# Kernel tuning notes

Measured on AMD Instinct MI355X. Metric: run time of the kernel, lower is better.

The kernel has to match this reference:

```python
import jax, jax.numpy as jnp
import numpy as np

EMBED_DIM = 768
FF_MULT = 4
HIDDEN = EMBED_DIM * FF_MULT
BATCH, SEQ = 32, 1024
EPS = 1e-6


def rmsnorm(x, g):
    # RMSNorm over last dim with learned scale g
    return x * jax.lax.rsqrt(jnp.mean(x * x, axis=-1, keepdims=True) + EPS) * g


def act_quant(x):
    # per-token int8 absmax quantization (BitNet b1.58)
    scale = 127.0 / jnp.clip(jnp.max(jnp.abs(x), axis=-1, keepdims=True), 1e-5, None)
    return jnp.clip(jnp.round(x * scale), -128.0, 127.0) / scale


def weight_quant(w):
    # per-tensor ternary (1.58-bit) absmean quantization
    scale = 1.0 / jnp.clip(jnp.mean(jnp.abs(w)), 1e-5, None)
    return jnp.clip(jnp.round(w * scale), -1.0, 1.0) / scale


def bitlinear(x, w, g):
    xn = rmsnorm(x, g)
    # straight-through estimator: forward uses quantized values
    xq = xn + jax.lax.stop_gradient(act_quant(xn) - xn)
    wq = w + jax.lax.stop_gradient(weight_quant(w) - w)
    return jnp.einsum('bsd,fd->bsf', xq, wq)


def setup_inputs() -> dict:
    key = jax.random.key(0)
    k1, k2, k3 = jax.random.split(key, 3)
    x = jax.random.normal(k1, (BATCH, SEQ, EMBED_DIM), dtype=jnp.float32)
    w1 = jax.random.normal(k2, (HIDDEN, EMBED_DIM), dtype=jnp.float32) * 0.02
    w2 = jax.random.normal(k3, (EMBED_DIM, HIDDEN), dtype=jnp.float32) * 0.02
    g1 = jnp.ones((EMBED_DIM,), dtype=jnp.float32)
    g2 = jnp.ones((HIDDEN,), dtype=jnp.float32)
    return {"x": x, "w1": w1, "g1": g1, "w2": w2, "g2": g2}


def reference(x, w1, g1, w2, g2):
    # BitFeedForward: BitLinear -> GELU (exact, matches nn.GELU) -> BitLinear
    # Dropout(p=0.0) is identity.
    h = jax.nn.gelu(bitlinear(x, w1, g1), approximate=False)
    return bitlinear(h, w2, g2)
```

## Files before the change

### kernel.cpp

```cpp
#include <hip/hip_runtime.h>
#include <hip/hip_bf16.h>
#include <hip/hip_fp16.h>
#include <math.h>

#define TOKENS 32768
#define EMBED  768
#define HIDDEN 3072
#define WELEMS (EMBED*HIDDEN)

typedef __attribute__((ext_vector_type(4))) int i32x4;
typedef __attribute__((ext_vector_type(4))) signed char i8x4;
typedef signed char i8;

__device__ __forceinline__ float wave_reduce_sum(float v) {
    for (int o = 32; o > 0; o >>= 1) v += __shfl_down(v, o);
    return v;
}
__device__ __forceinline__ float wave_reduce_max(float v) {
    for (int o = 32; o > 0; o >>= 1) v = fmaxf(v, __shfl_down(v, o));
    return v;
}

__device__ __forceinline__ float gelu_fast(float v) {
    const float z  = fabsf(v) * 0.70710678118654752440f;
    const float t  = __builtin_amdgcn_rcpf(fmaf(0.3275911f, z, 1.0f));
    float p = fmaf(1.061405429f, t, -1.453152027f);
    p = fmaf(p, t, 1.421413741f);
    p = fmaf(p, t, -0.284496736f);
    p = fmaf(p, t, 0.254829592f);
    p = p * t;
    const float e   = __expf(-z * z);
    const float erf = fmaf(-p, e, 1.0f);
    const float se  = (v >= 0.f) ? erf : -erf;
    return 0.5f * v * (1.0f + se);
}

__global__ __launch_bounds__(256) void k_abs_partial(const float* __restrict__ w,
                                                     float* __restrict__ out, int n) {
    float s = 0.f;
    for (int i = blockIdx.x * 256 + threadIdx.x; i < n; i += gridDim.x * 256)
        s += fabsf(w[i]);
    __shared__ float red[4];
    s = wave_reduce_sum(s);
    if ((threadIdx.x & 63) == 0) red[threadIdx.x >> 6] = s;
    __syncthreads();
    if (threadIdx.x == 0) out[blockIdx.x] = red[0] + red[1] + red[2] + red[3];
}

__global__ __launch_bounds__(256) void k_finalize(const float* __restrict__ p,
                                                  float* __restrict__ m) {
    __shared__ float r1[4], r2[4];
    float s1 = 0.f, s2 = 0.f;
    for (int i = threadIdx.x; i < 512; i += 256) { s1 += p[i]; s2 += p[512 + i]; }
    s1 = wave_reduce_sum(s1); s2 = wave_reduce_sum(s2);
    if ((threadIdx.x & 63) == 0) { r1[threadIdx.x >> 6] = s1; r2[threadIdx.x >> 6] = s2; }
    __syncthreads();
    if (threadIdx.x == 0) {
        float m1 = (r1[0] + r1[1] + r1[2] + r1[3]) / (float)WELEMS;
        float m2 = (r2[0] + r2[1] + r2[2] + r2[3]) / (float)WELEMS;
        m[0] = fmaxf(m1, 1e-5f);
        m[1] = fmaxf(m2, 1e-5f);
    }
}

__global__ __launch_bounds__(256) void k_quant_w(const float* __restrict__ w,
                                                 i8* __restrict__ wq,
                                                 const float* __restrict__ mp, int n) {
    const float inv = 1.0f / mp[0];
    for (int i = blockIdx.x * 256 + threadIdx.x; i < n; i += gridDim.x * 256) {
        float q = rintf(w[i] * inv);
        q = fminf(1.f, fmaxf(-1.f, q));
        wq[i] = (i8)(int)q;
    }
}

template <int D>
__global__ __launch_bounds__(256) void k_rms_quant_f32(const float* __restrict__ x,
                                                       const float* __restrict__ g,
                                                       i8* __restrict__ xq,
                                                       float* __restrict__ sc) {
    constexpr int NV = D / 4;
    constexpr int IT = (NV + 255) / 256;
    __shared__ float reds[4], redm[4];
    const int t = blockIdx.x;
    const float4* xp = reinterpret_cast<const float4*>(x + (size_t)t * D);
    const float4* gp = reinterpret_cast<const float4*>(g);
    float4 xg[IT];
    float ssq = 0.f, amax = 0.f;
#pragma unroll
    for (int i = 0; i < IT; ++i) {
        const int idx = i * 256 + (int)threadIdx.x;
        const bool act = (NV % 256 == 0) || (idx < NV);
        if (act) {
            float4 v = xp[idx];
            float4 gv = gp[idx];
            ssq += v.x * v.x + v.y * v.y + v.z * v.z + v.w * v.w;
            xg[i].x = v.x * gv.x; xg[i].y = v.y * gv.y;
            xg[i].z = v.z * gv.z; xg[i].w = v.w * gv.w;
            amax = fmaxf(amax, fmaxf(fmaxf(fabsf(xg[i].x), fabsf(xg[i].y)),
                                     fmaxf(fabsf(xg[i].z), fabsf(xg[i].w))));
        } else {
            xg[i].x = xg[i].y = xg[i].z = xg[i].w = 0.f;
        }
    }
    ssq = wave_reduce_sum(ssq);
    amax = wave_reduce_max(amax);
    if ((threadIdx.x & 63) == 0) { reds[threadIdx.x >> 6] = ssq; redm[threadIdx.x >> 6] = amax; }
    __syncthreads();
    const float S = reds[0] + reds[1] + reds[2] + reds[3];
    const float A = fmaxf(fmaxf(redm[0], redm[1]), fmaxf(redm[2], redm[3]));
    const float rs = (float)(1.0 / sqrt((double)S / D + 1e-6));
    const float an = fmaxf(A * rs, 1e-5f);
    const float qs = rs * (127.0f / an);
    if (threadIdx.x == 0) sc[t] = an * (1.0f / 127.0f);
    i8x4* op = reinterpret_cast<i8x4*>(xq + (size_t)t * D);
#pragma unroll
    for (int i = 0; i < IT; ++i) {
        const int idx = i * 256 + (int)threadIdx.x;
        const bool act = (NV % 256 == 0) || (idx < NV);
        if (act) {
            i8x4 r;
            r[0] = (i8)(int)fminf(127.f, fmaxf(-128.f, rintf(xg[i].x * qs)));
            r[1] = (i8)(int)fminf(127.f, fmaxf(-128.f, rintf(xg[i].y * qs)));
            r[2] = (i8)(int)fminf(127.f, fmaxf(-128.f, rintf(xg[i].z * qs)));
            r[3] = (i8)(int)fminf(127.f, fmaxf(-128.f, rintf(xg[i].w * qs)));
            op[idx] = r;
        }
    }
}

template <int D>
__global__ __launch_bounds__(256) void k_rms_quant_f16(const __half* __restrict__ x,
                                                       const float* __restrict__ g,
                                                       i8* __restrict__ xq,
                                                       float* __restrict__ sc) {
    constexpr int NV = D / 8;
    constexpr int IT = (NV + 255) / 256;
    __shared__ float reds[4], redm[4];
    const int t = blockIdx.x;
    const int4* xp = reinterpret_cast<const int4*>(x + (size_t)t * D);
    const float4* gp = reinterpret_cast<const float4*>(g);
    float xg[IT][8];
    float ssq = 0.f, amax = 0.f;
#pragma unroll
    for (int i = 0; i < IT; ++i) {
        const int idx = i * 256 + (int)threadIdx.x;
        const bool act = (NV % 256 == 0) || (idx < NV);
        if (act) {
            int4 raw = xp[idx];
            const __half2* hp = reinterpret_cast<const __half2*>(&raw);
            float4 g0 = gp[idx * 2];
            float4 g1 = gp[idx * 2 + 1];
            float gv[8] = {g0.x, g0.y, g0.z, g0.w, g1.x, g1.y, g1.z, g1.w};
#pragma unroll
            for (int j = 0; j < 4; ++j) {
                float2 f = __half22float2(hp[j]);
                float a0 = f.x, a1 = f.y;
                ssq += a0 * a0 + a1 * a1;
                xg[i][j * 2]     = a0 * gv[j * 2];
                xg[i][j * 2 + 1] = a1 * gv[j * 2 + 1];
                amax = fmaxf(amax, fmaxf(fabsf(xg[i][j * 2]), fabsf(xg[i][j * 2 + 1])));
            }
        } else {
#pragma unroll
            for (int j = 0; j < 8; ++j) xg[i][j] = 0.f;
        }
    }
    ssq = wave_reduce_sum(ssq);
    amax = wave_reduce_max(amax);
    if ((threadIdx.x & 63) == 0) { reds[threadIdx.x >> 6] = ssq; redm[threadIdx.x >> 6] = amax; }
    __syncthreads();
    const float S = reds[0] + reds[1] + reds[2] + reds[3];
    const float A = fmaxf(fmaxf(redm[0], redm[1]), fmaxf(redm[2], redm[3]));
    const float rs = (float)(1.0 / sqrt((double)S / D + 1e-6));
    const float an = fmaxf(A * rs, 1e-5f);
    const float qs = rs * (127.0f / an);
    if (threadIdx.x == 0) sc[t] = an * (1.0f / 127.0f);
    i8x4* op = reinterpret_cast<i8x4*>(xq + (size_t)t * D);
#pragma unroll
    for (int i = 0; i < IT; ++i) {
        const int idx = i * 256 + (int)threadIdx.x;
        const bool act = (NV % 256 == 0) || (idx < NV);
        if (act) {
            i8x4 r0, r1;
#pragma unroll
            for (int j = 0; j < 4; ++j)
                r0[j] = (i8)(int)fminf(127.f, fmaxf(-128.f, rintf(xg[i][j] * qs)));
#pragma unroll
            for (int j = 0; j < 4; ++j)
                r1[j] = (i8)(int)fminf(127.f, fmaxf(-128.f, rintf(xg[i][4 + j] * qs)));
            op[idx * 2]     = r0;
            op[idx * 2 + 1] = r1;
        }
    }
}

template <bool GELU, typename OutT>
__global__ __launch_bounds__(512, 4) void k_gemm_i8(const i8* __restrict__ A,
                                                    const i8* __restrict__ B,
                                                    OutT* __restrict__ C,
                                                    const float* __restrict__ rsc,
                                                    const float* __restrict__ msc,
                                                    int nbx, int N, int K) {
    __shared__ i8 As[128 * 128];
    __shared__ i8 Bs[256 * 128];
    const int nwg = (int)gridDim.x;
    const int id  = (int)blockIdx.x;
    const int q = nwg >> 3, r = nwg & 7;
    const int xcd = id & 7, sub = id >> 3;
    const int swz = (xcd < r ? xcd * (q + 1) : r * (q + 1) + (xcd - r) * q) + sub;
    const int bx = swz % nbx;
    const int by = swz / nbx;

    const int tid  = threadIdx.x;
    const int lane = tid & 63;
    const int wave = tid >> 6;
    const int wr = wave >> 2, wc = wave & 3;
    const size_t rowBase = (size_t)by * 128;
    const size_t colBase = (size_t)bx * 256;
    const float ms = msc[0];

    i32x4 acc[4][4] = {};

    const int srow = tid >> 3;
    const int cc   = tid & 7;
    const int gcol = (cc ^ (srow & 7)) * 16;
    const i8* gA0 = A + (rowBase + srow) * (size_t)K + gcol;
    const i8* gB0 = B + (colBase + srow) * (size_t)K + gcol;
    const int lOff = srow * 128 + cc * 16;

    const int frow = lane & 15;
    const int fko  = (lane >> 4) * 16;
    const int rswz = (frow & 7) << 4;

    for (int k0 = 0; k0 < K; k0 += 128) {
#pragma unroll
        for (int r2 = 0; r2 < 2; ++r2)
            __builtin_amdgcn_global_load_lds(
                (const __attribute__((address_space(1))) void*)(gA0 + (size_t)r2 * 64 * K + k0),
                (__attribute__((address_space(3))) void*)(&As[lOff + r2 * 64 * 128]), 16, 0, 0);
#pragma unroll
        for (int r4 = 0; r4 < 4; ++r4)
            __builtin_amdgcn_global_load_lds(
                (const __attribute__((address_space(1))) void*)(gB0 + (size_t)r4 * 64 * K + k0),
                (__attribute__((address_space(3))) void*)(&Bs[lOff + r4 * 64 * 128]), 16, 0, 0);
        __syncthreads();
#pragma unroll
        for (int ks = 0; ks < 2; ++ks) {
            i32x4 af[4], bv[4];
#pragma unroll
            for (int mi = 0; mi < 4; ++mi)
                af[mi] = *(const i32x4*)(&As[(wr * 64 + mi * 16 + frow) * 128
                                             + ((ks * 64 + fko) ^ rswz)]);
#pragma unroll
            for (int ni = 0; ni < 4; ++ni)
                bv[ni] = *(const i32x4*)(&Bs[(wc * 64 + ni * 16 + frow) * 128
                                             + ((ks * 64 + fko) ^ rswz)]);
#pragma unroll
            for (int mi = 0; mi < 4; ++mi)
#pragma unroll
                for (int ni = 0; ni < 4; ++ni)
                    acc[mi][ni] = __builtin_amdgcn_mfma_i32_16x16x64_i8(
                        af[mi], bv[ni], acc[mi][ni], 0, 0, 0);
        }
        __syncthreads();
    }

    const int ccol = lane & 15;
    const int crg  = lane >> 4;
#pragma unroll
    for (int mi = 0; mi < 4; ++mi) {
#pragma unroll
        for (int i = 0; i < 4; ++i) {
            size_t row = rowBase + wr * 64 + mi * 16 + crg * 4 + i;
            float rscale = rsc[row] * ms;
#pragma unroll
            for (int ni = 0; ni < 4; ++ni) {
                size_t col = colBase + wc * 64 + ni * 16 + ccol;
                float v = (float)acc[mi][ni][i] * rscale;
                if (GELU) v = gelu_fast(v);
                C[row * (size_t)N + col] = (OutT)v;
            }
        }
    }
}

extern "C" void kernel_launch(void* const* d_in, const int* in_sizes, int n_in,
                              void* d_out, int out_size, void* d_ws, size_t ws_size,
                              hipStream_t stream) {
    const float* x  = (const float*)d_in[0];
    const float* w1 = (const float*)d_in[1];
    const float* g1 = (const float*)d_in[2];
    const float* w2 = (const float*)d_in[3];
    const float* g2 = (const float*)d_in[4];
    float* out = (float*)d_out;

    char* ws = (char*)d_ws;
    float* partials = (float*)ws;
    float* mvals    = (float*)(ws + 4096);
    float* a        = (float*)(ws + 4352);
    float* b        = (float*)(ws + 135424);
    i8*    wq1      = (i8*)(ws + 266496);
    i8*    wq2      = (i8*)(ws + 2625792);
    const size_t FIXED = 4985088;
    char* chunkMem = ws + FIXED;

    const size_t PER_TOK = 768 + 6144 + 3072;
    size_t avail = (ws_size > FIXED) ? (ws_size - FIXED) : 0;
    long long ch = (long long)(avail / PER_TOK);
    ch &= ~255LL;
    if (ch < 256) ch = 256;
    if (ch > TOKENS) ch = TOKENS;
    const int CH = (int)ch;

    k_abs_partial<<<512, 256, 0, stream>>>(w1, partials, WELEMS);
    k_abs_partial<<<512, 256, 0, stream>>>(w2, partials + 512, WELEMS);
    k_finalize<<<1, 256, 0, stream>>>(partials, mvals);
    k_quant_w<<<2048, 256, 0, stream>>>(w1, wq1, mvals + 0, WELEMS);
    k_quant_w<<<2048, 256, 0, stream>>>(w2, wq2, mvals + 1, WELEMS);

    for (int base = 0; base < TOKENS; base += CH) {
        const int rows = (TOKENS - base < CH) ? (TOKENS - base) : CH;
        i8*     xqc = (i8*)chunkMem;
        __half* hc  = (__half*)(chunkMem + (size_t)CH * 768);
        i8*     hqc = (i8*)(chunkMem + (size_t)CH * 768 + (size_t)CH * 6144);

        const int nby = rows / 128;
        const int nbx1 = HIDDEN / 256;
        const int nbx2 = EMBED / 256;

        k_rms_quant_f32<EMBED><<<rows, 256, 0, stream>>>(
            x + (size_t)base * EMBED, g1, xqc, a + base);
        k_gemm_i8<true, __half><<<nbx1 * nby, 512, 0, stream>>>(
            xqc, wq1, hc, a + base, mvals + 0, nbx1, HIDDEN, EMBED);
        k_rms_quant_f16<HIDDEN><<<rows, 256, 0, stream>>>(
            hc, g2, hqc, b + base);
        k_gemm_i8<false, float><<<nbx2 * nby, 512, 0, stream>>>(
            hqc, wq2, out + (size_t)base * EMBED, b + base, mvals + 1, nbx2, EMBED, HIDDEN);
    }
}
```

Measured before the change: 365.2 us.

## Double-buffer int8 GEMM LDS tiles with 128x128 blocks and 256 threads

```diff
diff --git a/kernel.cpp b/kernel.cpp
--- a/kernel.cpp
+++ b/kernel.cpp
@@ -196,14 +196,15 @@
 }
 
 template <bool GELU, typename OutT>
-__global__ __launch_bounds__(512, 4) void k_gemm_i8(const i8* __restrict__ A,
+__global__ __launch_bounds__(256, 2) void k_gemm_i8(const i8* __restrict__ A,
                                                     const i8* __restrict__ B,
                                                     OutT* __restrict__ C,
                                                     const float* __restrict__ rsc,
                                                     const float* __restrict__ msc,
                                                     int nbx, int N, int K) {
-    __shared__ i8 As[128 * 128];
-    __shared__ i8 Bs[256 * 128];
+    __shared__ i8 As[2][128 * 128];
+    __shared__ i8 Bs[2][128 * 128];
+
     const int nwg = (int)gridDim.x;
     const int id  = (int)blockIdx.x;
     const int q = nwg >> 3, r = nwg & 7;
@@ -215,9 +216,9 @@
     const int tid  = threadIdx.x;
     const int lane = tid & 63;
     const int wave = tid >> 6;
-    const int wr = wave >> 2, wc = wave & 3;
+    const int wr = wave >> 1, wc = wave & 1;
     const size_t rowBase = (size_t)by * 128;
-    const size_t colBase = (size_t)bx * 256;
+    const size_t colBase = (size_t)bx * 128;
     const float ms = msc[0];
 
     i32x4 acc[4][4] = {};
@@ -233,38 +234,59 @@
     const int fko  = (lane >> 4) * 16;
     const int rswz = (frow & 7) << 4;
 
-    for (int k0 = 0; k0 < K; k0 += 128) {
-#pragma unroll
-        for (int r2 = 0; r2 < 2; ++r2)
-            __builtin_amdgcn_global_load_lds(
-                (const __attribute__((address_space(1))) void*)(gA0 + (size_t)r2 * 64 * K + k0),
-                (__attribute__((address_space(3))) void*)(&As[lOff + r2 * 64 * 128]), 16, 0, 0);
-#pragma unroll
-        for (int r4 = 0; r4 < 4; ++r4)
-            __builtin_amdgcn_global_load_lds(
-                (const __attribute__((address_space(1))) void*)(gB0 + (size_t)r4 * 64 * K + k0),
-                (__attribute__((address_space(3))) void*)(&Bs[lOff + r4 * 64 * 128]), 16, 0, 0);
-        __syncthreads();
+    const int nt = K >> 7;
+
+#define STAGE(kk, buf)                                                                   \
+    {                                                                                    \
+        const int _k0 = (kk) << 7;                                                       \
+        _Pragma("unroll")                                                                \
+        for (int _r = 0; _r < 4; ++_r) {                                                 \
+            __builtin_amdgcn_global_load_lds(                                            \
+                (const __attribute__((address_space(1))) void*)(gA0 + (size_t)_r * 32 * K + _k0), \
+                (__attribute__((address_space(3))) void*)(&As[buf][lOff + _r * 32 * 128]), 16, 0, 0); \
+            __builtin_amdgcn_global_load_lds(                                            \
+                (const __attribute__((address_space(1))) void*)(gB0 + (size_t)_r * 32 * K + _k0), \
+                (__attribute__((address_space(3))) void*)(&Bs[buf][lOff + _r * 32 * 128]), 16, 0, 0); \
+        }                                                                                \
+    }
+
+    STAGE(0, 0);
+
+    for (int t = 0; t < nt; ++t) {
+        const int cur = t & 1;
+        if (t + 1 < nt) {
+            STAGE(t + 1, cur ^ 1);
+            asm volatile("s_waitcnt vmcnt(8)" ::: "memory");
+        } else {
+            asm volatile("s_waitcnt vmcnt(0)" ::: "memory");
+        }
+        __builtin_amdgcn_s_barrier();
+        __builtin_amdgcn_sched_barrier(0);
 #pragma unroll
         for (int ks = 0; ks < 2; ++ks) {
             i32x4 af[4], bv[4];
 #pragma unroll
             for (int mi = 0; mi < 4; ++mi)
-                af[mi] = *(const i32x4*)(&As[(wr * 64 + mi * 16 + frow) * 128
-                                             + ((ks * 64 + fko) ^ rswz)]);
+                af[mi] = *(const i32x4*)(&As[cur][(wr * 64 + mi * 16 + frow) * 128
+                                                  + ((ks * 64 + fko) ^ rswz)]);
 #pragma unroll
             for (int ni = 0; ni < 4; ++ni)
-                bv[ni] = *(const i32x4*)(&Bs[(wc * 64 + ni * 16 + frow) * 128
-                                             + ((ks * 64 + fko) ^ rswz)]);
+                bv[ni] = *(const i32x4*)(&Bs[cur][(wc * 64 + ni * 16 + frow) * 128
+                                                  + ((ks * 64 + fko) ^ rswz)]);
+            __builtin_amdgcn_s_setprio(1);
 #pragma unroll
             for (int mi = 0; mi < 4; ++mi)
 #pragma unroll
                 for (int ni = 0; ni < 4; ++ni)
                     acc[mi][ni] = __builtin_amdgcn_mfma_i32_16x16x64_i8(
                         af[mi], bv[ni], acc[mi][ni], 0, 0, 0);
-        }
-        __syncthreads();
-    }
+            __builtin_amdgcn_s_setprio(0);
+        }
+        __builtin_amdgcn_sched_barrier(0);
+        __builtin_amdgcn_s_barrier();
+        __builtin_amdgcn_sched_barrier(0);
+    }
+#undef STAGE
 
     const int ccol = lane & 15;
     const int crg  = lane >> 4;
@@ -326,16 +348,16 @@
         i8*     hqc = (i8*)(chunkMem + (size_t)CH * 768 + (size_t)CH * 6144);
 
         const int nby = rows / 128;
-        const int nbx1 = HIDDEN / 256;
-        const int nbx2 = EMBED / 256;
+        const int nbx1 = HIDDEN / 128;
+        const int nbx2 = EMBED / 128;
 
         k_rms_quant_f32<EMBED><<<rows, 256, 0, stream>>>(
             x + (size_t)base * EMBED, g1, xqc, a + base);
-        k_gemm_i8<true, __half><<<nbx1 * nby, 512, 0, stream>>>(
+        k_gemm_i8<true, __half><<<nbx1 * nby, 256, 0, stream>>>(
             xqc, wq1, hc, a + base, mvals + 0, nbx1, HIDDEN, EMBED);
         k_rms_quant_f16<HIDDEN><<<rows, 256, 0, stream>>>(
             hc, g2, hqc, b + base);
-        k_gemm_i8<false, float><<<nbx2 * nby, 512, 0, stream>>>(
+        k_gemm_i8<false, float><<<nbx2 * nby, 256, 0, stream>>>(
             hqc, wq2, out + (size_t)base * EMBED, b + base, mvals + 1, nbx2, EMBED, HIDDEN);
     }
 }
```

Result: slower. 392.8 us (+7.5%).

## Double-buffer int8 GEMM with 256x256 tiles and phased MFMA/load interleaving

Applied to the files above, without the earlier changes.

```diff
diff --git a/kernel.cpp b/kernel.cpp
--- a/kernel.cpp
+++ b/kernel.cpp
@@ -196,83 +196,138 @@
 }
 
 template <bool GELU, typename OutT>
-__global__ __launch_bounds__(512, 4) void k_gemm_i8(const i8* __restrict__ A,
-                                                    const i8* __restrict__ B,
-                                                    OutT* __restrict__ C,
-                                                    const float* __restrict__ rsc,
-                                                    const float* __restrict__ msc,
-                                                    int nbx, int N, int K) {
-    __shared__ i8 As[128 * 128];
-    __shared__ i8 Bs[256 * 128];
+__global__ __launch_bounds__(512, 2) void k_gemm8(const i8* __restrict__ A,
+                                                  const i8* __restrict__ B,
+                                                  OutT* __restrict__ C,
+                                                  const float* __restrict__ rsc,
+                                                  const float* __restrict__ msc,
+                                                  int nbx, int N, int K) {
+    __shared__ i8 As[2][256 * 128];
+    __shared__ i8 Bs[2][256 * 128];
+
     const int nwg = (int)gridDim.x;
     const int id  = (int)blockIdx.x;
-    const int q = nwg >> 3, r = nwg & 7;
+    const int q8 = nwg >> 3, r8 = nwg & 7;
     const int xcd = id & 7, sub = id >> 3;
-    const int swz = (xcd < r ? xcd * (q + 1) : r * (q + 1) + (xcd - r) * q) + sub;
+    const int swz = (xcd < r8 ? xcd * (q8 + 1) : r8 * (q8 + 1) + (xcd - r8) * q8) + sub;
     const int bx = swz % nbx;
     const int by = swz / nbx;
 
-    const int tid  = threadIdx.x;
+    const int tid  = (int)threadIdx.x;
     const int lane = tid & 63;
     const int wave = tid >> 6;
-    const int wr = wave >> 2, wc = wave & 3;
-    const size_t rowBase = (size_t)by * 128;
+    const int wr = wave >> 2;
+    const int wc = wave & 3;
+    const size_t rowBase = (size_t)by * 256;
     const size_t colBase = (size_t)bx * 256;
     const float ms = msc[0];
 
-    i32x4 acc[4][4] = {};
+    i32x4 acc[8][4] = {};
 
     const int srow = tid >> 3;
     const int cc   = tid & 7;
-    const int gcol = (cc ^ (srow & 7)) * 16;
-    const i8* gA0 = A + (rowBase + srow) * (size_t)K + gcol;
-    const i8* gB0 = B + (colBase + srow) * (size_t)K + gcol;
-    const int lOff = srow * 128 + cc * 16;
+    const int gch  = (cc ^ (srow & 7)) * 16;
+    const i8* gA0 = A + (rowBase + srow) * (size_t)K + gch;
+    const i8* gB0 = B + (colBase + srow) * (size_t)K + gch;
 
     const int frow = lane & 15;
     const int fko  = (lane >> 4) * 16;
     const int rswz = (frow & 7) << 4;
 
-    for (int k0 = 0; k0 < K; k0 += 128) {
-#pragma unroll
-        for (int r2 = 0; r2 < 2; ++r2)
-            __builtin_amdgcn_global_load_lds(
-                (const __attribute__((address_space(1))) void*)(gA0 + (size_t)r2 * 64 * K + k0),
-                (__attribute__((address_space(3))) void*)(&As[lOff + r2 * 64 * 128]), 16, 0, 0);
-#pragma unroll
-        for (int r4 = 0; r4 < 4; ++r4)
-            __builtin_amdgcn_global_load_lds(
-                (const __attribute__((address_space(1))) void*)(gB0 + (size_t)r4 * 64 * K + k0),
-                (__attribute__((address_space(3))) void*)(&Bs[lOff + r4 * 64 * 128]), 16, 0, 0);
-        __syncthreads();
-#pragma unroll
-        for (int ks = 0; ks < 2; ++ks) {
-            i32x4 af[4], bv[4];
-#pragma unroll
-            for (int mi = 0; mi < 4; ++mi)
-                af[mi] = *(const i32x4*)(&As[(wr * 64 + mi * 16 + frow) * 128
-                                             + ((ks * 64 + fko) ^ rswz)]);
-#pragma unroll
-            for (int ni = 0; ni < 4; ++ni)
-                bv[ni] = *(const i32x4*)(&Bs[(wc * 64 + ni * 16 + frow) * 128
-                                             + ((ks * 64 + fko) ^ rswz)]);
-#pragma unroll
-            for (int mi = 0; mi < 4; ++mi)
-#pragma unroll
-                for (int ni = 0; ni < 4; ++ni)
-                    acc[mi][ni] = __builtin_amdgcn_mfma_i32_16x16x64_i8(
-                        af[mi], bv[ni], acc[mi][ni], 0, 0, 0);
-        }
-        __syncthreads();
-    }
+    const int nt = K >> 7;
+    const int niters = nt >> 1;
+
+#define STG(TS, GP, buf, h, kk)                                                \
+    { _Pragma("unroll")                                                        \
+      for (int _r = 0; _r < 2; ++_r)                                           \
+          __builtin_amdgcn_global_load_lds(                                    \
+              (const __attribute__((address_space(1))) void*)                  \
+                  (GP + (size_t)((h) * 128 + _r * 64) * K + ((size_t)(kk) << 7)), \
+              (__attribute__((address_space(3))) void*)                        \
+                  (&TS[buf][((h) * 128 + _r * 64) * 128 + tid * 16]),          \
+              16, 0, 0); }
+
+    STG(Bs, gB0, 0, 0, 0) STG(Bs, gB0, 0, 1, 0)
+    STG(As, gA0, 0, 0, 0) STG(As, gA0, 0, 1, 0)
+    STG(Bs, gB0, 1, 0, 1) STG(Bs, gB0, 1, 1, 1)
+    asm volatile("s_waitcnt vmcnt(4)" ::: "memory");
+    __builtin_amdgcn_s_barrier();
+    __builtin_amdgcn_sched_barrier(0);
+
+    i32x4 bv[8];
+
+#define LOADBV(cb)                                                             \
+    _Pragma("unroll")                                                          \
+    for (int ni = 0; ni < 4; ++ni)                                             \
+        _Pragma("unroll")                                                      \
+        for (int ks = 0; ks < 2; ++ks)                                         \
+            bv[ni * 2 + ks] = *(const i32x4*)(&Bs[cb][(wc * 64 + ni * 16 + frow) * 128 \
+                                                      + ((ks * 64 + fko) ^ rswz)]);
+
+#define PHASE(cb, q, STAGE_CODE, TAIL_CODE)                                    \
+    {                                                                          \
+        i32x4 a0[2], a1[2];                                                    \
+        _Pragma("unroll")                                                      \
+        for (int ks = 0; ks < 2; ++ks) {                                       \
+            a0[ks] = *(const i32x4*)(&As[cb][(wr * 128 + (2 * (q)) * 16 + frow) * 128 \
+                                             + ((ks * 64 + fko) ^ rswz)]);     \
+            a1[ks] = *(const i32x4*)(&As[cb][(wr * 128 + (2 * (q) + 1) * 16 + frow) * 128 \
+                                             + ((ks * 64 + fko) ^ rswz)]);     \
+        }                                                                      \
+        STAGE_CODE                                                             \
+        __builtin_amdgcn_s_barrier();                                          \
+        __builtin_amdgcn_sched_barrier(0);                                     \
+        __builtin_amdgcn_s_setprio(1);                                         \
+        _Pragma("unroll")                                                      \
+        for (int ks = 0; ks < 2; ++ks)                                         \
+            _Pragma("unroll")                                                  \
+            for (int ni = 0; ni < 4; ++ni) {                                   \
+                acc[2 * (q)][ni] = __builtin_amdgcn_mfma_i32_16x16x64_i8(      \
+                    a0[ks], bv[ni * 2 + ks], acc[2 * (q)][ni], 0, 0, 0);       \
+                acc[2 * (q) + 1][ni] = __builtin_amdgcn_mfma_i32_16x16x64_i8(  \
+                    a1[ks], bv[ni * 2 + ks], acc[2 * (q) + 1][ni], 0, 0, 0);   \
+            }                                                                  \
+        __builtin_amdgcn_s_setprio(0);                                         \
+        __builtin_amdgcn_sched_barrier(0);                                     \
+        TAIL_CODE                                                              \
+        __builtin_amdgcn_s_barrier();                                          \
+        __builtin_amdgcn_sched_barrier(0);                                     \
+    }
+
+    for (int it = 0; it < niters; ++it) {
+        const int tO  = 2 * it + 1;
+        const int tE2 = 2 * it + 2;
+        const int tO2 = 2 * it + 3;
+        const bool hE2 = (tE2 < nt);
+        const bool hO2 = (tO2 < nt);
+
+        LOADBV(0)
+        PHASE(0, 0, { STG(As, gA0, 1, 0, tO) }, {})
+        PHASE(0, 1, { STG(As, gA0, 1, 1, tO)
+                      if (hE2) STG(Bs, gB0, 0, 0, tE2) }, {})
+        PHASE(0, 2, { if (hE2) STG(Bs, gB0, 0, 1, tE2) }, {})
+        PHASE(0, 3, {},
+              { if (hE2) { asm volatile("s_waitcnt vmcnt(4)" ::: "memory"); }
+                else     { asm volatile("s_waitcnt vmcnt(0)" ::: "memory"); } })
+        LOADBV(1)
+        PHASE(1, 0, { if (hE2) STG(As, gA0, 0, 0, tE2) }, {})
+        PHASE(1, 1, { if (hE2) STG(As, gA0, 0, 1, tE2)
+                      if (hO2) STG(Bs, gB0, 1, 0, tO2) }, {})
+        PHASE(1, 2, { if (hO2) STG(Bs, gB0, 1, 1, tO2) }, {})
+        PHASE(1, 3, {},
+              { if (hE2) { asm volatile("s_waitcnt vmcnt(4)" ::: "memory"); } })
+    }
+#undef PHASE
+#undef LOADBV
+#undef STG
 
     const int ccol = lane & 15;
     const int crg  = lane >> 4;
 #pragma unroll
-    for (int mi = 0; mi < 4; ++mi) {
+    for (int mi = 0; mi < 8; ++mi) {
 #pragma unroll
         for (int i = 0; i < 4; ++i) {
-            size_t row = rowBase + wr * 64 + mi * 16 + crg * 4 + i;
+            size_t row = rowBase + wr * 128 + mi * 16 + crg * 4 + i;
             float rscale = rsc[row] * ms;
 #pragma unroll
             for (int ni = 0; ni < 4; ++ni) {
@@ -325,17 +380,17 @@
         __half* hc  = (__half*)(chunkMem + (size_t)CH * 768);
         i8*     hqc = (i8*)(chunkMem + (size_t)CH * 768 + (size_t)CH * 6144);
 
-        const int nby = rows / 128;
+        const int nby  = rows / 256;
         const int nbx1 = HIDDEN / 256;
         const int nbx2 = EMBED / 256;
 
         k_rms_quant_f32<EMBED><<<rows, 256, 0, stream>>>(
             x + (size_t)base * EMBED, g1, xqc, a + base);
-        k_gemm_i8<true, __half><<<nbx1 * nby, 512, 0, stream>>>(
+        k_gemm8<true, __half><<<nbx1 * nby, 512, 0, stream>>>(
             xqc, wq1, hc, a + base, mvals + 0, nbx1, HIDDEN, EMBED);
         k_rms_quant_f16<HIDDEN><<<rows, 256, 0, stream>>>(
             hc, g2, hqc, b + base);
-        k_gemm_i8<false, float><<<nbx2 * nby, 512, 0, stream>>>(
+        k_gemm8<false, float><<<nbx2 * nby, 512, 0, stream>>>(
             hqc, wq2, out + (size_t)base * EMBED, b + base, mvals + 1, nbx2, EMBED, HIDDEN);
     }
 }
```

New measurement: 387.1 us. 1.06x slower.
